# Kernel tuning notes

Measured on AMD Instinct MI355X. Metric: run time of the kernel, lower is better.

The kernel has to match this reference:

```python
import jax, jax.numpy as jnp
import numpy as np

BETA = 0.25
DECAY = 0.99
EPS = 1e-05
K = 1024        # num_codebook_vectors
D = 256         # latent_dim


def setup_inputs() -> dict:
    key = jax.random.key(0)
    k1, k2, k3 = jax.random.split(key, 3)
    return {
        "z": jax.random.normal(k1, (32, D, 32, 32), dtype=jnp.float32),
        "embedding": jax.random.normal(k2, (K, D), dtype=jnp.float32),
        "ema_cluster_size": jnp.zeros((K,), dtype=jnp.float32),
        "ema_w": jax.random.normal(k3, (K, D), dtype=jnp.float32),
    }


def reference(z, embedding, ema_cluster_size, ema_w):
    B, C, H, W = z.shape
    zp = jnp.transpose(z, (0, 2, 3, 1))            # [B,H,W,C]
    zf = zp.reshape(-1, C)                          # [N, D], N = B*H*W

    # squared L2 distances: ||z||^2 + ||e||^2 - 2 z e^T  -> [N, K]
    d = (jnp.sum(zf * zf, axis=1, keepdims=True)
         + jnp.sum(embedding * embedding, axis=1)
         - 2.0 * (zf @ embedding.T))
    idx = jnp.argmin(d, axis=1)                     # [N]

    # one-hot @ embedding == gather of codebook rows
    z_q = embedding[idx].reshape(zp.shape)          # [B,H,W,C]

    # EMA codebook update (training branch)
    counts = jnp.zeros((K,), dtype=zf.dtype).at[idx].add(1.0)   # encodings.sum(0)
    cs = ema_cluster_size * DECAY + (1.0 - DECAY) * counts
    n = jnp.sum(cs)
    cs = (cs + EPS) / (n + K * EPS) * n             # Laplace smoothing
    dw = jax.ops.segment_sum(zf, idx, num_segments=K)           # encodings.T @ zf
    new_ema_w = ema_w * DECAY + (1.0 - DECAY) * dw
    new_embedding = new_ema_w / cs[:, None]

    # commitment loss + straight-through estimator
    e_latent_loss = jnp.mean((jax.lax.stop_gradient(z_q) - zp) ** 2)
    loss = BETA * e_latent_loss
    z_q_st = zp + jax.lax.stop_gradient(z_q - zp)
    z_q_out = jnp.transpose(z_q_st, (0, 3, 1, 2))   # [B,C,H,W]

    return z_q_out, idx[:, None], loss, new_embedding, cs, new_ema_w
```

## Files before the change

kernel.cpp:

```cpp
#include <hip/hip_runtime.h>

typedef unsigned long long ull;
typedef __attribute__((ext_vector_type(8))) short bf16x8;
typedef __attribute__((ext_vector_type(4))) float f32x4;
typedef __attribute__((ext_vector_type(8))) unsigned short u16x8;

#define DECAY 0.99f
#define BETA 0.25f
#define EPSV 1e-5f
#define EPSGAP 0.0625f
#define THR3 0.03125f

#define Dd 256
#define Kk 1024
#define Nn 32768
#define ZELEM 8388608

__device__ __forceinline__ unsigned short f2bf(float f) {
    unsigned int x = __float_as_uint(f);
    x += 0x7FFFu + ((x >> 16) & 1u);
    return (unsigned short)(x >> 16);
}
__device__ __forceinline__ float bf2f(unsigned short b) {
    return __uint_as_float(((unsigned int)b) << 16);
}
__device__ __forceinline__ unsigned mono(unsigned b) {
    return b ^ (((int)b >> 31) | 0x80000000u);
}
__device__ __forceinline__ float unmono(unsigned m) {
    unsigned b = (m & 0x80000000u) ? (m ^ 0x80000000u) : ~m;
    return __uint_as_float(b);
}
__device__ __forceinline__ unsigned umin32(unsigned a, unsigned b) { return a < b ? a : b; }
__device__ __forceinline__ unsigned umax32(unsigned a, unsigned b) { return a > b ? a : b; }
__device__ __forceinline__ ull umin64(ull a, ull b) { return a < b ? a : b; }
__device__ __forceinline__ ull umax64(ull a, ull b) { return a > b ? a : b; }

__global__ __launch_bounds__(256) void prep_e_kernel(
        const float* __restrict__ emb, unsigned short* __restrict__ ehg,
        unsigned short* __restrict__ elg, float* __restrict__ esq,
        int* __restrict__ hist, int* __restrict__ flagcnt,
        float* __restrict__ loss_fix, float* __restrict__ nsum,
        const float* __restrict__ ema_cs, float* __restrict__ dwr, int nrep) {
    const int nsub = blockIdx.x;
    const int t = threadIdx.x;
    {
        const int per = nrep * 512;
        float4* dst = (float4*)(dwr + (size_t)nsub * per);
        const int n4 = per >> 2;
        for (int j = t; j < n4; j += 256) dst[j] = make_float4(0.f, 0.f, 0.f, 0.f);
    }
    if (nsub < 64) {
        if (t < 16) hist[nsub * 16 + t] = 0;
        if (nsub == 0 && t == 16) flagcnt[0] = 0;
        if (nsub == 0 && t == 17) loss_fix[0] = 0.0f;
        if (nsub == 0 && t == 18) flagcnt[1] = 0;
        #pragma unroll
        for (int it = 0; it < 2; ++it) {
            const int item = it * 256 + t;
            const int kc = item >> 6, lane = item & 63;
            const int quad = lane >> 4, nl = lane & 15;
            const float* ep = emb + (size_t)(nsub * 16 + nl) * Dd + kc * 32 + quad * 8;
            const float4 a = *(const float4*)ep;
            const float4 b4 = *(const float4*)(ep + 4);
            const float v[8] = {a.x, a.y, a.z, a.w, b4.x, b4.y, b4.z, b4.w};
            u16x8 hi, lo;
            #pragma unroll
            for (int j = 0; j < 8; ++j) {
                const unsigned short h = f2bf(v[j]);
                hi[j] = h;
                lo[j] = f2bf(v[j] - bf2f(h));
            }
            const size_t off = ((size_t)(nsub * 8 + kc) * 64 + lane) * 8;
            *(u16x8*)&ehg[off] = hi;
            *(u16x8*)&elg[off] = lo;
        }
        {
            const int nl = t >> 4, seg = t & 15;
            const float* ep = emb + (size_t)(nsub * 16 + nl) * Dd + seg * 16;
            float s = 0.0f;
            #pragma unroll
            for (int j = 0; j < 4; ++j) {
                const float4 v4 = *(const float4*)(ep + j * 4);
                s += v4.x * v4.x + v4.y * v4.y + v4.z * v4.z + v4.w * v4.w;
            }
            #pragma unroll
            for (int d = 1; d < 16; d <<= 1) s += __shfl_xor(s, d);
            if (seg == 0) esq[nsub * 16 + nl] = s;
        }
    } else if (nsub == 64) {
        __shared__ float wred[4];
        const int w = t >> 6, lane = t & 63;
        float s = ema_cs[t] + ema_cs[t + 256] + ema_cs[t + 512] + ema_cs[t + 768];
        #pragma unroll
        for (int d = 32; d > 0; d >>= 1) s += __shfl_xor(s, d);
        if (lane == 0) wred[w] = s;
        __syncthreads();
        if (t == 0)
            nsum[0] = DECAY * (wred[0] + wred[1] + wred[2] + wred[3])
                      + (1.0f - DECAY) * (float)Nn;
    }
}

__global__ __launch_bounds__(256) void dist_kernel(
        const float* __restrict__ z, const unsigned short* __restrict__ ehg,
        const unsigned short* __restrict__ elg, const float* __restrict__ esq,
        const float* __restrict__ emb,
        float* __restrict__ zq, float* __restrict__ dwr, int repmask,
        int* __restrict__ idx_i, float* __restrict__ idx_f,
        int* __restrict__ hist, int* __restrict__ flagcnt,
        int* __restrict__ listA, int* __restrict__ kkA,
        float* __restrict__ valA, int* __restrict__ listB,
        float* __restrict__ valB, float* __restrict__ loss_p) {
    __shared__ __align__(16) unsigned char smem[72704];
    __shared__ int kidx[64];
    unsigned short* zh = (unsigned short*)smem;
    unsigned short* zl = (unsigned short*)(smem + 32768);
    ull* mb   = (ull*)(smem + 65536);
    ull* ms   = (ull*)(smem + 67584);
    float* zsqp = (float*)(smem + 69632);
    ull* mt   = (ull*)(smem + 70656);
    float* eldsf = (float*)smem;

    const int t = threadIdx.x, w = t >> 6, L = t & 63;
    const int quad = L >> 4, lr = L & 15;
    const int m0 = blockIdx.x * 64;
    const int b = m0 >> 10, hw0 = m0 & 1023;

    {
        const int c0 = w * 64;
        const float* zp = z + (size_t)b * 262144 + hw0 + L;
        float s = 0.0f;
        #pragma unroll
        for (int cg = 0; cg < 8; ++cg) {
            float v[8];
            #pragma unroll
            for (int j = 0; j < 8; ++j)
                v[j] = zp[(size_t)(c0 + cg * 8 + j) * 1024];
            u16x8 hi, lo;
            #pragma unroll
            for (int j = 0; j < 8; ++j) {
                s = fmaf(v[j], v[j], s);
                const unsigned short h = f2bf(v[j]);
                hi[j] = h;
                lo[j] = f2bf(v[j] - bf2f(h));
            }
            const int chunk = ((c0 >> 3) + cg) ^ (L & 7);
            *(u16x8*)&zh[L * 256 + chunk * 8] = hi;
            *(u16x8*)&zl[L * 256 + chunk * 8] = lo;
        }
        zsqp[L * 4 + w] = s;
    }
    __syncthreads();

    const unsigned short* ehw = ehg + (size_t)(w * 1024 + L) * 8;
    const unsigned short* elw = elg + (size_t)(w * 1024 + L) * 8;

    unsigned bb[16], ss[16], tt[16];
    #pragma unroll
    for (int i = 0; i < 16; ++i) { bb[i] = 0xFFFFFFFFu; ss[i] = 0xFFFFFFFFu; tt[i] = 0xFFFFFFFFu; }

    bf16x8 Bh[2][2], Bl[2][2];
    #pragma unroll
    for (int ni = 0; ni < 2; ++ni) {
        Bh[0][ni] = *(const bf16x8*)(ehw + (size_t)ni * 4096);
        Bl[0][ni] = *(const bf16x8*)(elw + (size_t)ni * 4096);
    }
    bf16x8 Ah[2][4], Al[2][4];
    #pragma unroll
    for (int mi = 0; mi < 4; ++mi) {
        const int chunk = quad ^ (lr & 7);
        const int o = (mi * 16 + lr) * 256 + chunk * 8;
        Ah[0][mi] = *(const bf16x8*)&zh[o];
        Al[0][mi] = *(const bf16x8*)&zl[o];
    }

    for (int nt = 0; nt < 8; ++nt) {
        f32x4 acc[4][2];
        #pragma unroll
        for (int mi = 0; mi < 4; ++mi)
            #pragma unroll
            for (int ni = 0; ni < 2; ++ni) acc[mi][ni] = (f32x4){0.f, 0.f, 0.f, 0.f};

        #pragma unroll
        for (int kc = 0; kc < 8; ++kc) {
            const int cur = kc & 1, nxt = cur ^ 1;
            const int nkc = (kc + 1) & 7;
            const int nnt = (kc == 7) ? ((nt + 1) & 7) : nt;
            #pragma unroll
            for (int ni = 0; ni < 2; ++ni) {
                const size_t o = (size_t)nnt * 32768 + (size_t)ni * 4096 + (size_t)nkc * 512;
                Bh[nxt][ni] = *(const bf16x8*)(ehw + o);
                Bl[nxt][ni] = *(const bf16x8*)(elw + o);
            }
            #pragma unroll
            for (int mi = 0; mi < 4; ++mi) {
                const int chunk = (nkc * 4 + quad) ^ (lr & 7);
                const int o = (mi * 16 + lr) * 256 + chunk * 8;
                Ah[nxt][mi] = *(const bf16x8*)&zh[o];
                Al[nxt][mi] = *(const bf16x8*)&zl[o];
            }
            __builtin_amdgcn_s_setprio(1);
            #pragma unroll
            for (int mi = 0; mi < 4; ++mi)
                #pragma unroll
                for (int ni = 0; ni < 2; ++ni) {
                    acc[mi][ni] = __builtin_amdgcn_mfma_f32_16x16x32_bf16(Ah[cur][mi], Bh[cur][ni], acc[mi][ni], 0, 0, 0);
                    acc[mi][ni] = __builtin_amdgcn_mfma_f32_16x16x32_bf16(Ah[cur][mi], Bl[cur][ni], acc[mi][ni], 0, 0, 0);
                    acc[mi][ni] = __builtin_amdgcn_mfma_f32_16x16x32_bf16(Al[cur][mi], Bh[cur][ni], acc[mi][ni], 0, 0, 0);
                }
            __builtin_amdgcn_s_setprio(0);
        }
        const int q0 = nt * 8 + w * 2;
        const float e0b = esq[q0 * 16 + lr] + 512.0f;
        const float e1b = esq[(q0 + 1) * 16 + lr] + 512.0f;
        #pragma unroll
        for (int mi = 0; mi < 4; ++mi)
            #pragma unroll
            for (int reg = 0; reg < 4; ++reg) {
                const int i = mi * 4 + reg;
                #pragma unroll
                for (int ni = 0; ni < 2; ++ni) {
                    const float val = fmaf(-2.0f, acc[mi][ni][reg], ni ? e1b : e0b);
                    const unsigned pk = (__float_as_uint(val) & 0xFFFFFFC0u) | (unsigned)(q0 + ni);
                    const unsigned m1 = umin32(bb[i], pk), M1 = umax32(bb[i], pk);
                    const unsigned m2 = umin32(ss[i], M1), M2 = umax32(ss[i], M1);
                    const unsigned m3 = umin32(tt[i], M2);
                    bb[i] = m1; ss[i] = m2; tt[i] = m3;
                }
            }
    }

    #pragma unroll
    for (int mi = 0; mi < 4; ++mi)
        #pragma unroll
        for (int reg = 0; reg < 4; ++reg) {
            const int i = mi * 4 + reg;
            ull b2 = ((ull)(bb[i] & 0xFFFFFFC0u) << 14) | (ull)((bb[i] & 63u) * 16 + lr);
            ull s2 = ((ull)(ss[i] & 0xFFFFFFC0u) << 14) | (ull)((ss[i] & 63u) * 16 + lr);
            ull t2 = ((ull)(tt[i] & 0xFFFFFFC0u) << 14) | (ull)((tt[i] & 63u) * 16 + lr);
            #pragma unroll
            for (int d = 1; d < 16; d <<= 1) {
                const ull ob = __shfl_xor(b2, d);
                const ull os = __shfl_xor(s2, d);
                const ull ot = __shfl_xor(t2, d);
                const ull x1 = umin64(b2, ob), y1 = umax64(b2, ob);
                const ull x2 = umin64(s2, os), y2 = umax64(s2, os);
                const ull c2 = umin64(y1, x2);
                const ull t1 = umax64(y1, x2);
                const ull c3 = umin64(t1, umin64(y2, umin64(t2, ot)));
                b2 = x1; s2 = c2; t2 = c3;
            }
            if (lr == 0) {
                const int row = mi * 16 + quad * 4 + reg;
                mb[w * 64 + row] = b2;
                ms[w * 64 + row] = s2;
                mt[w * 64 + row] = t2;
            }
        }
    __syncthreads();

    if (t < 64) {
        ull b2 = mb[t], s2 = ms[t], t2 = mt[t];
        #pragma unroll
        for (int ww = 1; ww < 4; ++ww) {
            const ull ob = mb[ww * 64 + t], os = ms[ww * 64 + t], ot = mt[ww * 64 + t];
            const ull x1 = umin64(b2, ob), y1 = umax64(b2, ob);
            const ull x2 = umin64(s2, os), y2 = umax64(s2, os);
            const ull c2 = umin64(y1, x2);
            const ull t1 = umax64(y1, x2);
            const ull c3 = umin64(t1, umin64(y2, umin64(t2, ot)));
            b2 = x1; s2 = c2; t2 = c3;
        }
        const int k1 = (int)(b2 & 16383ull);
        const int k2 = (int)(s2 & 16383ull);
        const float v1 = __uint_as_float((unsigned)(b2 >> 14)) - 512.0f;
        const float v2 = __uint_as_float((unsigned)(s2 >> 14)) - 512.0f;
        const float v3 = __uint_as_float((unsigned)(t2 >> 14)) - 512.0f;
        idx_i[m0 + t] = k1;
        idx_f[m0 + t] = (float)k1;
        kidx[t] = k1;
        atomicAdd(&hist[k1], 1);
        if (v2 - v1 < EPSGAP) {
            if (v3 - v1 < THR3) {
                const int pos = atomicAdd(&flagcnt[1], 1);
                listB[pos] = m0 + t;
                valB[pos] = v1;
            } else {
                const int pos = atomicAdd(&flagcnt[0], 1);
                listA[pos] = m0 + t;
                kkA[pos] = k1 | (k2 << 16);
                valA[pos] = v1;
            }
        }
        float lp = v1 + zsqp[t * 4] + zsqp[t * 4 + 1] + zsqp[t * 4 + 2] + zsqp[t * 4 + 3];
        #pragma unroll
        for (int d = 32; d > 0; d >>= 1) lp += __shfl_down(lp, d);
        if (t == 0) loss_p[blockIdx.x] = lp;
    }
    __syncthreads();

    for (int pr = w; pr < 64; pr += 4) {
        const float* er = emb + (size_t)kidx[pr] * Dd;
        #pragma unroll
        for (int g = 0; g < 4; ++g)
            eldsf[pr * 257 + g * 64 + L] = er[g * 64 + L];
    }
    __syncthreads();

    {
        const int g = t & 15;
        const int cl = t >> 4;
        float* zqb = zq + (size_t)b * 262144 + hw0 + g * 4;
        #pragma unroll
        for (int pass = 0; pass < 16; ++pass) {
            const int c = pass * 16 + cl;
            float4 v;
            v.x = eldsf[(g * 4 + 0) * 257 + c];
            v.y = eldsf[(g * 4 + 1) * 257 + c];
            v.z = eldsf[(g * 4 + 2) * 257 + c];
            v.w = eldsf[(g * 4 + 3) * 257 + c];
            *(float4*)(zqb + (size_t)c * 1024) = v;
        }
    }

    {
        const int c = t;
        const float* zcol = z + (size_t)b * 262144 + (size_t)c * 1024 + hw0;
        float* dwb = dwr + (size_t)(blockIdx.x & repmask) * (Kk * Dd);
        #pragma unroll 4
        for (int p = 0; p < 64; ++p) {
            atomicAdd(&dwb[(size_t)kidx[p] * Dd + c], zcol[p]);
        }
    }
}

__global__ __launch_bounds__(256) void fixup_kernel(
        const float* __restrict__ z, const float* __restrict__ emb,
        const float* __restrict__ esq, const int* __restrict__ flagcnt,
        const int* __restrict__ listA, const int* __restrict__ kkA,
        const float* __restrict__ valA, const int* __restrict__ listB,
        const float* __restrict__ valB,
        int* __restrict__ idx_i, float* __restrict__ idx_f,
        int* __restrict__ hist, float* __restrict__ loss_fix,
        float* __restrict__ zq, float* __restrict__ dw) {
    __shared__ float zrow[256];
    __shared__ float red1[4], red2[4];
    __shared__ ull red[256];
    __shared__ int s_pair[2];
    const int t = threadIdx.x;
    const int w = t >> 6, lane = t & 63;

    const int totalA = flagcnt[0];
    for (int fi = blockIdx.x; fi < totalA; fi += 512) {
        const int n = listA[fi];
        const int b = n >> 10, hw = n & 1023;
        const int kk = kkA[fi];
        const int k1 = kk & 0xFFFF, k2 = kk >> 16;
        __syncthreads();
        zrow[t] = z[(size_t)b * 262144 + (size_t)t * 1024 + hw];
        __syncthreads();
        const float zv = zrow[t];
        float c1 = zv * emb[(size_t)k1 * Dd + t];
        float c2 = zv * emb[(size_t)k2 * Dd + t];
        #pragma unroll
        for (int d = 32; d > 0; d >>= 1) {
            c1 += __shfl_xor(c1, d);
            c2 += __shfl_xor(c2, d);
        }
        if (lane == 0) { red1[w] = c1; red2[w] = c2; }
        __syncthreads();
        if (t == 0) {
            const float d1 = esq[k1] - 2.0f * (red1[0] + red1[1] + red1[2] + red1[3]);
            const float d2 = esq[k2] - 2.0f * (red2[0] + red2[1] + red2[2] + red2[3]);
            const ull p1 = ((ull)mono(__float_as_uint(d1)) << 32) | (unsigned)k1;
            const ull p2 = ((ull)mono(__float_as_uint(d2)) << 32) | (unsigned)k2;
            const ull pb = p1 < p2 ? p1 : p2;
            const int knew = (int)(unsigned)(pb & 0xFFFFFFFFull);
            const float vnew = unmono((unsigned)(pb >> 32));
            const int kold = idx_i[n];
            s_pair[0] = kold;
            s_pair[1] = knew;
            if (knew != kold) {
                idx_i[n] = knew;
                idx_f[n] = (float)knew;
                atomicSub(&hist[kold], 1);
                atomicAdd(&hist[knew], 1);
            }
            atomicAdd(loss_fix, vnew - valA[fi]);
        }
        __syncthreads();
        const int kold = s_pair[0], knew = s_pair[1];
        if (knew != kold) {
            atomicAdd(&dw[(size_t)kold * Dd + t], -zv);
            atomicAdd(&dw[(size_t)knew * Dd + t], zv);
            zq[(size_t)b * 262144 + (size_t)t * 1024 + hw] = emb[(size_t)knew * Dd + t];
        }
    }

    const int totalB = flagcnt[1];
    for (int fi = blockIdx.x; fi < totalB; fi += 512) {
        const int n = listB[fi];
        const int b = n >> 10, hw = n & 1023;
        __syncthreads();
        zrow[t] = z[(size_t)b * 262144 + (size_t)t * 1024 + hw];
        __syncthreads();
        ull best = ~0ull;
        #pragma unroll
        for (int kc = 0; kc < 4; ++kc) {
            const int k = t * 4 + kc;
            const float* ep = emb + (size_t)k * Dd;
            float dot = 0.0f;
            #pragma unroll 8
            for (int c4 = 0; c4 < 64; ++c4) {
                const float4 e4 = *(const float4*)(ep + c4 * 4);
                const float4 z4 = *(const float4*)&zrow[c4 * 4];
                dot = fmaf(z4.x, e4.x, dot);
                dot = fmaf(z4.y, e4.y, dot);
                dot = fmaf(z4.z, e4.z, dot);
                dot = fmaf(z4.w, e4.w, dot);
            }
            const float val = esq[k] - 2.0f * dot;
            const ull pk = ((ull)mono(__float_as_uint(val)) << 32) | (unsigned)k;
            if (pk < best) best = pk;
        }
        red[t] = best;
        __syncthreads();
        for (int s = 128; s > 0; s >>= 1) {
            if (t < s) { if (red[t + s] < red[t]) red[t] = red[t + s]; }
            __syncthreads();
        }
        if (t == 0) {
            const int knew = (int)(unsigned)(red[0] & 0xFFFFFFFFull);
            const float vnew = unmono((unsigned)(red[0] >> 32));
            const int kold = idx_i[n];
            s_pair[0] = kold;
            s_pair[1] = knew;
            if (knew != kold) {
                idx_i[n] = knew;
                idx_f[n] = (float)knew;
                atomicSub(&hist[kold], 1);
                atomicAdd(&hist[knew], 1);
            }
            atomicAdd(loss_fix, vnew - valB[fi]);
        }
        __syncthreads();
        const int kold = s_pair[0], knew = s_pair[1];
        if (knew != kold) {
            const float zv = zrow[t];
            atomicAdd(&dw[(size_t)kold * Dd + t], -zv);
            atomicAdd(&dw[(size_t)knew * Dd + t], zv);
            zq[(size_t)b * 262144 + (size_t)t * 1024 + hw] = emb[(size_t)knew * Dd + t];
        }
    }
}

__global__ __launch_bounds__(256) void finalize2_kernel(
        const float* __restrict__ ema_w, const float* __restrict__ dwr,
        int nrep, const int* __restrict__ hist,
        const float* __restrict__ ema_cs, const float* __restrict__ nsum,
        const float* __restrict__ loss_p, const float* __restrict__ loss_fix,
        float* __restrict__ cs_out, float* __restrict__ loss_out,
        float* __restrict__ new_emb_out, float* __restrict__ new_ema_w_out) {
    const int k = blockIdx.x;
    const int t = threadIdx.x;
    const float n = nsum[0];
    const float csr = ema_cs[k] * DECAY + (1.0f - DECAY) * (float)hist[k];
    const float cs = (csr + EPSV) / (n + (float)Kk * EPSV) * n;
    if (t == 0) cs_out[k] = cs;
    const int i = k * 256 + t;
    float s = 0.0f;
    for (int r = 0; r < nrep; ++r) s += dwr[(size_t)r * (Kk * Dd) + i];
    const float nw = ema_w[i] * DECAY + (1.0f - DECAY) * s;
    new_ema_w_out[i] = nw;
    new_emb_out[i]   = nw / cs;
    if (k == 0) {
        __shared__ float wred[4];
        const int w = t >> 6, lane = t & 63;
        float r2 = loss_p[t] + loss_p[t + 256];
        #pragma unroll
        for (int d = 32; d > 0; d >>= 1) r2 += __shfl_xor(r2, d);
        if (lane == 0) wred[w] = r2;
        __syncthreads();
        if (t == 0)
            loss_out[0] = BETA * (wred[0] + wred[1] + wred[2] + wred[3]
                                  + loss_fix[0]) / (float)ZELEM;
    }
}

extern "C" void kernel_launch(void* const* d_in, const int* in_sizes, int n_in,
                              void* d_out, int out_size, void* d_ws, size_t ws_size,
                              hipStream_t stream) {
    const float* z      = (const float*)d_in[0];
    const float* emb    = (const float*)d_in[1];
    const float* ema_cs = (const float*)d_in[2];
    const float* ema_w  = (const float*)d_in[3];

    float* out = (float*)d_out;
    float* zq_out        = out;
    float* idx_out_f     = out + 8388608;
    float* loss_out      = out + 8421376;
    float* new_emb_out   = out + 8421377;
    float* cs_out        = out + 8683521;
    float* new_ema_w_out = out + 8684545;

    int*   idx_i    = (int*)d_ws;
    int*   flagcnt  = idx_i + 32768;
    float* loss_fix = (float*)(flagcnt + 16);
    int*   listA    = (int*)(loss_fix + 16);
    float* valA     = (float*)(listA + 32768);
    int*   kkA      = (int*)(valA + 32768);
    int*   listB    = kkA + 32768;
    float* valB     = (float*)(listB + 32768);
    int*   hist     = (int*)(valB + 32768);
    float* esq      = (float*)(hist + 1024);
    float* loss_p   = esq + 1024;
    float* nsum     = loss_p + 512;
    unsigned short* ehg = (unsigned short*)(nsum + 16);
    unsigned short* elg = ehg + 262144;
    size_t dwr_off = ((size_t)((char*)(elg + 262144) - (char*)d_ws) + 255) & ~(size_t)255;
    float* dwr = (float*)((char*)d_ws + dwr_off);
    const size_t repbytes = (size_t)Kk * Dd * 4;
    size_t rem = (ws_size > dwr_off) ? ws_size - dwr_off : 0;
    int nrep = 1;
    while (nrep < 8 && (size_t)(nrep * 2) * repbytes <= rem) nrep <<= 1;

    prep_e_kernel<<<512, 256, 0, stream>>>(emb, ehg, elg, esq, hist, flagcnt,
                                           loss_fix, nsum, ema_cs, dwr, nrep);
    dist_kernel<<<Nn / 64, 256, 0, stream>>>(z, ehg, elg, esq, emb, zq_out,
                                             dwr, nrep - 1, idx_i, idx_out_f,
                                             hist, flagcnt, listA, kkA, valA,
                                             listB, valB, loss_p);
    fixup_kernel<<<512, 256, 0, stream>>>(z, emb, esq, flagcnt, listA, kkA,
                                          valA, listB, valB, idx_i, idx_out_f,
                                          hist, loss_fix, zq_out, dwr);
    finalize2_kernel<<<Kk, 256, 0, stream>>>(ema_w, dwr, nrep, hist, ema_cs,
                                             nsum, loss_p, loss_fix, cs_out,
                                             loss_out, new_emb_out,
                                             new_ema_w_out);
}
```

Measured before the change: 213.2 us.

## Replace atomic scatter of dw with per-code gather over transposed z

Removes the atomicAdd-based segment sum and histogram from the distance kernel. Instead, the distance kernel writes a row-major copy of z into the zq output buffer. A new per-codebook kernel scans all indices, builds a shared-memory list of matching rows and sums them with no atomics, producing the counts and dw deterministically. A separate gather kernel then writes z_q after the fixups, which removes the fixup kernel's corrective atomics. In exchange, every one of the 1024 blocks scans all 32768 indices, and the dist kernel writes an extra 32 MB transposed copy.

```diff
diff --git a/kernel.cpp b/kernel.cpp
--- a/kernel.cpp
+++ b/kernel.cpp
@@ -39,19 +39,11 @@
 __global__ __launch_bounds__(256) void prep_e_kernel(
         const float* __restrict__ emb, unsigned short* __restrict__ ehg,
         unsigned short* __restrict__ elg, float* __restrict__ esq,
-        int* __restrict__ hist, int* __restrict__ flagcnt,
-        float* __restrict__ loss_fix, float* __restrict__ nsum,
-        const float* __restrict__ ema_cs, float* __restrict__ dwr, int nrep) {
+        int* __restrict__ flagcnt, float* __restrict__ loss_fix,
+        float* __restrict__ nsum, const float* __restrict__ ema_cs) {
     const int nsub = blockIdx.x;
     const int t = threadIdx.x;
-    {
-        const int per = nrep * 512;
-        float4* dst = (float4*)(dwr + (size_t)nsub * per);
-        const int n4 = per >> 2;
-        for (int j = t; j < n4; j += 256) dst[j] = make_float4(0.f, 0.f, 0.f, 0.f);
-    }
     if (nsub < 64) {
-        if (t < 16) hist[nsub * 16 + t] = 0;
         if (nsub == 0 && t == 16) flagcnt[0] = 0;
         if (nsub == 0 && t == 17) loss_fix[0] = 0.0f;
         if (nsub == 0 && t == 18) flagcnt[1] = 0;
@@ -88,7 +80,7 @@
             for (int d = 1; d < 16; d <<= 1) s += __shfl_xor(s, d);
             if (seg == 0) esq[nsub * 16 + nl] = s;
         }
-    } else if (nsub == 64) {
+    } else {
         __shared__ float wred[4];
         const int w = t >> 6, lane = t & 63;
         float s = ema_cs[t] + ema_cs[t + 256] + ema_cs[t + 512] + ema_cs[t + 768];
@@ -105,22 +97,19 @@
 __global__ __launch_bounds__(256) void dist_kernel(
         const float* __restrict__ z, const unsigned short* __restrict__ ehg,
         const unsigned short* __restrict__ elg, const float* __restrict__ esq,
-        const float* __restrict__ emb,
-        float* __restrict__ zq, float* __restrict__ dwr, int repmask,
+        float* __restrict__ zf,
         int* __restrict__ idx_i, float* __restrict__ idx_f,
-        int* __restrict__ hist, int* __restrict__ flagcnt,
+        int* __restrict__ flagcnt,
         int* __restrict__ listA, int* __restrict__ kkA,
         float* __restrict__ valA, int* __restrict__ listB,
         float* __restrict__ valB, float* __restrict__ loss_p) {
     __shared__ __align__(16) unsigned char smem[72704];
-    __shared__ int kidx[64];
     unsigned short* zh = (unsigned short*)smem;
     unsigned short* zl = (unsigned short*)(smem + 32768);
     ull* mb   = (ull*)(smem + 65536);
     ull* ms   = (ull*)(smem + 67584);
     float* zsqp = (float*)(smem + 69632);
     ull* mt   = (ull*)(smem + 70656);
-    float* eldsf = (float*)smem;
 
     const int t = threadIdx.x, w = t >> 6, L = t & 63;
     const int quad = L >> 4, lr = L & 15;
@@ -130,6 +119,7 @@
     {
         const int c0 = w * 64;
         const float* zp = z + (size_t)b * 262144 + hw0 + L;
+        float* zfp = zf + (size_t)(m0 + L) * 256 + c0;
         float s = 0.0f;
         #pragma unroll
         for (int cg = 0; cg < 8; ++cg) {
@@ -137,6 +127,8 @@
             #pragma unroll
             for (int j = 0; j < 8; ++j)
                 v[j] = zp[(size_t)(c0 + cg * 8 + j) * 1024];
+            *(float4*)(zfp + cg * 8)     = make_float4(v[0], v[1], v[2], v[3]);
+            *(float4*)(zfp + cg * 8 + 4) = make_float4(v[4], v[5], v[6], v[7]);
             u16x8 hi, lo;
             #pragma unroll
             for (int j = 0; j < 8; ++j) {
@@ -279,8 +271,6 @@
         const float v3 = __uint_as_float((unsigned)(t2 >> 14)) - 512.0f;
         idx_i[m0 + t] = k1;
         idx_f[m0 + t] = (float)k1;
-        kidx[t] = k1;
-        atomicAdd(&hist[k1], 1);
         if (v2 - v1 < EPSGAP) {
             if (v3 - v1 < THR3) {
                 const int pos = atomicAdd(&flagcnt[1], 1);
@@ -298,69 +288,28 @@
         for (int d = 32; d > 0; d >>= 1) lp += __shfl_down(lp, d);
         if (t == 0) loss_p[blockIdx.x] = lp;
     }
-    __syncthreads();
-
-    for (int pr = w; pr < 64; pr += 4) {
-        const float* er = emb + (size_t)kidx[pr] * Dd;
-        #pragma unroll
-        for (int g = 0; g < 4; ++g)
-            eldsf[pr * 257 + g * 64 + L] = er[g * 64 + L];
-    }
-    __syncthreads();
-
-    {
-        const int g = t & 15;
-        const int cl = t >> 4;
-        float* zqb = zq + (size_t)b * 262144 + hw0 + g * 4;
-        #pragma unroll
-        for (int pass = 0; pass < 16; ++pass) {
-            const int c = pass * 16 + cl;
-            float4 v;
-            v.x = eldsf[(g * 4 + 0) * 257 + c];
-            v.y = eldsf[(g * 4 + 1) * 257 + c];
-            v.z = eldsf[(g * 4 + 2) * 257 + c];
-            v.w = eldsf[(g * 4 + 3) * 257 + c];
-            *(float4*)(zqb + (size_t)c * 1024) = v;
-        }
-    }
-
-    {
-        const int c = t;
-        const float* zcol = z + (size_t)b * 262144 + (size_t)c * 1024 + hw0;
-        float* dwb = dwr + (size_t)(blockIdx.x & repmask) * (Kk * Dd);
-        #pragma unroll 4
-        for (int p = 0; p < 64; ++p) {
-            atomicAdd(&dwb[(size_t)kidx[p] * Dd + c], zcol[p]);
-        }
-    }
 }
 
 __global__ __launch_bounds__(256) void fixup_kernel(
-        const float* __restrict__ z, const float* __restrict__ emb,
+        const float* __restrict__ zf, const float* __restrict__ emb,
         const float* __restrict__ esq, const int* __restrict__ flagcnt,
         const int* __restrict__ listA, const int* __restrict__ kkA,
         const float* __restrict__ valA, const int* __restrict__ listB,
         const float* __restrict__ valB,
         int* __restrict__ idx_i, float* __restrict__ idx_f,
-        int* __restrict__ hist, float* __restrict__ loss_fix,
-        float* __restrict__ zq, float* __restrict__ dw) {
+        float* __restrict__ loss_fix) {
     __shared__ float zrow[256];
     __shared__ float red1[4], red2[4];
     __shared__ ull red[256];
-    __shared__ int s_pair[2];
     const int t = threadIdx.x;
     const int w = t >> 6, lane = t & 63;
 
     const int totalA = flagcnt[0];
     for (int fi = blockIdx.x; fi < totalA; fi += 512) {
         const int n = listA[fi];
-        const int b = n >> 10, hw = n & 1023;
         const int kk = kkA[fi];
         const int k1 = kk & 0xFFFF, k2 = kk >> 16;
-        __syncthreads();
-        zrow[t] = z[(size_t)b * 262144 + (size_t)t * 1024 + hw];
-        __syncthreads();
-        const float zv = zrow[t];
+        const float zv = zf[(size_t)n * Dd + t];
         float c1 = zv * emb[(size_t)k1 * Dd + t];
         float c2 = zv * emb[(size_t)k2 * Dd + t];
         #pragma unroll
@@ -368,6 +317,7 @@
             c1 += __shfl_xor(c1, d);
             c2 += __shfl_xor(c2, d);
         }
+        __syncthreads();
         if (lane == 0) { red1[w] = c1; red2[w] = c2; }
         __syncthreads();
         if (t == 0) {
@@ -378,32 +328,19 @@
             const ull pb = p1 < p2 ? p1 : p2;
             const int knew = (int)(unsigned)(pb & 0xFFFFFFFFull);
             const float vnew = unmono((unsigned)(pb >> 32));
-            const int kold = idx_i[n];
-            s_pair[0] = kold;
-            s_pair[1] = knew;
-            if (knew != kold) {
+            if (knew != k1) {
                 idx_i[n] = knew;
                 idx_f[n] = (float)knew;
-                atomicSub(&hist[kold], 1);
-                atomicAdd(&hist[knew], 1);
             }
             atomicAdd(loss_fix, vnew - valA[fi]);
-        }
-        __syncthreads();
-        const int kold = s_pair[0], knew = s_pair[1];
-        if (knew != kold) {
-            atomicAdd(&dw[(size_t)kold * Dd + t], -zv);
-            atomicAdd(&dw[(size_t)knew * Dd + t], zv);
-            zq[(size_t)b * 262144 + (size_t)t * 1024 + hw] = emb[(size_t)knew * Dd + t];
         }
     }
 
     const int totalB = flagcnt[1];
     for (int fi = blockIdx.x; fi < totalB; fi += 512) {
         const int n = listB[fi];
-        const int b = n >> 10, hw = n & 1023;
-        __syncthreads();
-        zrow[t] = z[(size_t)b * 262144 + (size_t)t * 1024 + hw];
+        __syncthreads();
+        zrow[t] = zf[(size_t)n * Dd + t];
         __syncthreads();
         ull best = ~0ull;
         #pragma unroll
@@ -434,44 +371,50 @@
             const int knew = (int)(unsigned)(red[0] & 0xFFFFFFFFull);
             const float vnew = unmono((unsigned)(red[0] >> 32));
             const int kold = idx_i[n];
-            s_pair[0] = kold;
-            s_pair[1] = knew;
             if (knew != kold) {
                 idx_i[n] = knew;
                 idx_f[n] = (float)knew;
-                atomicSub(&hist[kold], 1);
-                atomicAdd(&hist[knew], 1);
             }
             atomicAdd(loss_fix, vnew - valB[fi]);
         }
-        __syncthreads();
-        const int kold = s_pair[0], knew = s_pair[1];
-        if (knew != kold) {
-            const float zv = zrow[t];
-            atomicAdd(&dw[(size_t)kold * Dd + t], -zv);
-            atomicAdd(&dw[(size_t)knew * Dd + t], zv);
-            zq[(size_t)b * 262144 + (size_t)t * 1024 + hw] = emb[(size_t)knew * Dd + t];
-        }
-    }
-}
-
-__global__ __launch_bounds__(256) void finalize2_kernel(
-        const float* __restrict__ ema_w, const float* __restrict__ dwr,
-        int nrep, const int* __restrict__ hist,
-        const float* __restrict__ ema_cs, const float* __restrict__ nsum,
-        const float* __restrict__ loss_p, const float* __restrict__ loss_fix,
+    }
+}
+
+__global__ __launch_bounds__(256) void dwfin_kernel(
+        const int* __restrict__ idx, const float* __restrict__ zf,
+        const float* __restrict__ ema_w, const float* __restrict__ ema_cs,
+        const float* __restrict__ nsum, const float* __restrict__ loss_p,
+        const float* __restrict__ loss_fix,
         float* __restrict__ cs_out, float* __restrict__ loss_out,
         float* __restrict__ new_emb_out, float* __restrict__ new_ema_w_out) {
+    __shared__ int list[2048];
+    __shared__ int lcnt;
     const int k = blockIdx.x;
     const int t = threadIdx.x;
+    float acc = 0.0f;
+    int cnt = 0;
+    for (int seg = 0; seg < Nn; seg += 2048) {
+        __syncthreads();
+        if (t == 0) lcnt = 0;
+        __syncthreads();
+        #pragma unroll
+        for (int j = 0; j < 8; ++j) {
+            const int n = seg + j * 256 + t;
+            if (idx[n] == k) list[atomicAdd(&lcnt, 1)] = n;
+        }
+        __syncthreads();
+        const int m = lcnt;
+        cnt += m;
+        #pragma unroll 4
+        for (int i = 0; i < m; ++i)
+            acc += zf[(size_t)list[i] * Dd + t];
+    }
     const float n = nsum[0];
-    const float csr = ema_cs[k] * DECAY + (1.0f - DECAY) * (float)hist[k];
+    const float csr = ema_cs[k] * DECAY + (1.0f - DECAY) * (float)cnt;
     const float cs = (csr + EPSV) / (n + (float)Kk * EPSV) * n;
     if (t == 0) cs_out[k] = cs;
     const int i = k * 256 + t;
-    float s = 0.0f;
-    for (int r = 0; r < nrep; ++r) s += dwr[(size_t)r * (Kk * Dd) + i];
-    const float nw = ema_w[i] * DECAY + (1.0f - DECAY) * s;
+    const float nw = ema_w[i] * DECAY + (1.0f - DECAY) * acc;
     new_ema_w_out[i] = nw;
     new_emb_out[i]   = nw / cs;
     if (k == 0) {
@@ -486,6 +429,23 @@
             loss_out[0] = BETA * (wred[0] + wred[1] + wred[2] + wred[3]
                                   + loss_fix[0]) / (float)ZELEM;
     }
+}
+
+__global__ __launch_bounds__(256) void gather_kernel(
+        const float* __restrict__ emb, const int* __restrict__ idx,
+        float* __restrict__ zq_out) {
+    const int tid = blockIdx.x * 256 + threadIdx.x;
+    const int e0 = tid * 4;
+    const int c = (e0 >> 10) & 255;
+    const int b = e0 >> 18;
+    const int n0 = b * 1024 + (e0 & 1023);
+    const int4 j4 = *(const int4*)(idx + n0);
+    float4 e;
+    e.x = emb[(size_t)j4.x * Dd + c];
+    e.y = emb[(size_t)j4.y * Dd + c];
+    e.z = emb[(size_t)j4.z * Dd + c];
+    e.w = emb[(size_t)j4.w * Dd + c];
+    *(float4*)(zq_out + e0) = e;
 }
 
 extern "C" void kernel_launch(void* const* d_in, const int* in_sizes, int n_in,
@@ -512,30 +472,24 @@
     int*   kkA      = (int*)(valA + 32768);
     int*   listB    = kkA + 32768;
     float* valB     = (float*)(listB + 32768);
-    int*   hist     = (int*)(valB + 32768);
-    float* esq      = (float*)(hist + 1024);
+    float* esq      = valB + 32768;
     float* loss_p   = esq + 1024;
     float* nsum     = loss_p + 512;
     unsigned short* ehg = (unsigned short*)(nsum + 16);
     unsigned short* elg = ehg + 262144;
-    size_t dwr_off = ((size_t)((char*)(elg + 262144) - (char*)d_ws) + 255) & ~(size_t)255;
-    float* dwr = (float*)((char*)d_ws + dwr_off);
-    const size_t repbytes = (size_t)Kk * Dd * 4;
-    size_t rem = (ws_size > dwr_off) ? ws_size - dwr_off : 0;
-    int nrep = 1;
-    while (nrep < 8 && (size_t)(nrep * 2) * repbytes <= rem) nrep <<= 1;
-
-    prep_e_kernel<<<512, 256, 0, stream>>>(emb, ehg, elg, esq, hist, flagcnt,
-                                           loss_fix, nsum, ema_cs, dwr, nrep);
-    dist_kernel<<<Nn / 64, 256, 0, stream>>>(z, ehg, elg, esq, emb, zq_out,
-                                             dwr, nrep - 1, idx_i, idx_out_f,
-                                             hist, flagcnt, listA, kkA, valA,
-                                             listB, valB, loss_p);
-    fixup_kernel<<<512, 256, 0, stream>>>(z, emb, esq, flagcnt, listA, kkA,
+
+    float* zf = zq_out;
+
+    prep_e_kernel<<<65, 256, 0, stream>>>(emb, ehg, elg, esq, flagcnt,
+                                          loss_fix, nsum, ema_cs);
+    dist_kernel<<<Nn / 64, 256, 0, stream>>>(z, ehg, elg, esq, zf, idx_i,
+                                             idx_out_f, flagcnt, listA, kkA,
+                                             valA, listB, valB, loss_p);
+    fixup_kernel<<<512, 256, 0, stream>>>(zf, emb, esq, flagcnt, listA, kkA,
                                           valA, listB, valB, idx_i, idx_out_f,
-                                          hist, loss_fix, zq_out, dwr);
-    finalize2_kernel<<<Kk, 256, 0, stream>>>(ema_w, dwr, nrep, hist, ema_cs,
-                                             nsum, loss_p, loss_fix, cs_out,
-                                             loss_out, new_emb_out,
-                                             new_ema_w_out);
-}
+                                          loss_fix);
+    dwfin_kernel<<<Kk, 256, 0, stream>>>(idx_i, zf, ema_w, ema_cs, nsum,
+                                         loss_p, loss_fix, cs_out, loss_out,
+                                         new_emb_out, new_ema_w_out);
+    gather_kernel<<<ZELEM / 1024, 256, 0, stream>>>(emb, idx_i, zq_out);
+}
```

New measurement: 345.0 us. 61.8% more time.

## Fuse near-tie argmin refinement into distance kernel, drop fixup kernel

Applied to the files above, without the earlier changes.

Rows whose top-two or top-three split-bf16 distances are too close to call are now re-checked inside the distance kernel, using block-local shared lists and the z row already held in LDS as hi/lo bf16. This runs before idx, histogram, loss and the zq/dw scatter are written, so the separate fixup kernel with its global lists, atomics and correction scatters goes away, along with one launch. The cost is that a whole block waits on serial per-row refinement, including a full 1024-code scan for three-way ties, which can make some blocks uneven. The reconstructed z is hi+lo bf16, not the exact fp32 value.

```diff
diff --git a/kernel.cpp b/kernel.cpp
--- a/kernel.cpp
+++ b/kernel.cpp
@@ -39,8 +39,7 @@
 __global__ __launch_bounds__(256) void prep_e_kernel(
         const float* __restrict__ emb, unsigned short* __restrict__ ehg,
         unsigned short* __restrict__ elg, float* __restrict__ esq,
-        int* __restrict__ hist, int* __restrict__ flagcnt,
-        float* __restrict__ loss_fix, float* __restrict__ nsum,
+        int* __restrict__ hist, float* __restrict__ nsum,
         const float* __restrict__ ema_cs, float* __restrict__ dwr, int nrep) {
     const int nsub = blockIdx.x;
     const int t = threadIdx.x;
@@ -52,9 +51,6 @@
     }
     if (nsub < 64) {
         if (t < 16) hist[nsub * 16 + t] = 0;
-        if (nsub == 0 && t == 16) flagcnt[0] = 0;
-        if (nsub == 0 && t == 17) loss_fix[0] = 0.0f;
-        if (nsub == 0 && t == 18) flagcnt[1] = 0;
         #pragma unroll
         for (int it = 0; it < 2; ++it) {
             const int item = it * 256 + t;
@@ -108,24 +104,29 @@
         const float* __restrict__ emb,
         float* __restrict__ zq, float* __restrict__ dwr, int repmask,
         int* __restrict__ idx_i, float* __restrict__ idx_f,
-        int* __restrict__ hist, int* __restrict__ flagcnt,
-        int* __restrict__ listA, int* __restrict__ kkA,
-        float* __restrict__ valA, int* __restrict__ listB,
-        float* __restrict__ valB, float* __restrict__ loss_p) {
+        int* __restrict__ hist, float* __restrict__ loss_p) {
     __shared__ __align__(16) unsigned char smem[72704];
     __shared__ int kidx[64];
+    __shared__ float vv[64];
+    __shared__ int aList[64], bList[64];
+    __shared__ int acnt, bcnt;
+    __shared__ float red1[4], red2[4];
+    __shared__ ull bred[4];
     unsigned short* zh = (unsigned short*)smem;
     unsigned short* zl = (unsigned short*)(smem + 32768);
     ull* mb   = (ull*)(smem + 65536);
     ull* ms   = (ull*)(smem + 67584);
     float* zsqp = (float*)(smem + 69632);
     ull* mt   = (ull*)(smem + 70656);
+    float* zrowF = (float*)mb;
     float* eldsf = (float*)smem;
 
     const int t = threadIdx.x, w = t >> 6, L = t & 63;
     const int quad = L >> 4, lr = L & 15;
     const int m0 = blockIdx.x * 64;
     const int b = m0 >> 10, hw0 = m0 & 1023;
+
+    if (t == 0) { acnt = 0; bcnt = 0; }
 
     {
         const int c0 = w * 64;
@@ -277,23 +278,90 @@
         const float v1 = __uint_as_float((unsigned)(b2 >> 14)) - 512.0f;
         const float v2 = __uint_as_float((unsigned)(s2 >> 14)) - 512.0f;
         const float v3 = __uint_as_float((unsigned)(t2 >> 14)) - 512.0f;
-        idx_i[m0 + t] = k1;
-        idx_f[m0 + t] = (float)k1;
         kidx[t] = k1;
-        atomicAdd(&hist[k1], 1);
+        vv[t] = v1;
         if (v2 - v1 < EPSGAP) {
-            if (v3 - v1 < THR3) {
-                const int pos = atomicAdd(&flagcnt[1], 1);
-                listB[pos] = m0 + t;
-                valB[pos] = v1;
-            } else {
-                const int pos = atomicAdd(&flagcnt[0], 1);
-                listA[pos] = m0 + t;
-                kkA[pos] = k1 | (k2 << 16);
-                valA[pos] = v1;
-            }
-        }
-        float lp = v1 + zsqp[t * 4] + zsqp[t * 4 + 1] + zsqp[t * 4 + 2] + zsqp[t * 4 + 3];
+            if (v3 - v1 < THR3) bList[atomicAdd(&bcnt, 1)] = t;
+            else                aList[atomicAdd(&acnt, 1)] = t | (k2 << 8);
+        }
+    }
+    __syncthreads();
+
+    const int nA = acnt, nB = bcnt;
+    for (int i = 0; i < nA; ++i) {
+        const int e = aList[i];
+        const int p = e & 63, k2p = e >> 8;
+        const int k1p = kidx[p];
+        const int a = p * 256 + (((t >> 3) ^ (p & 7)) << 3) + (t & 7);
+        const float zv = bf2f(zh[a]) + bf2f(zl[a]);
+        float c1 = zv * emb[(size_t)k1p * Dd + t];
+        float c2 = zv * emb[(size_t)k2p * Dd + t];
+        #pragma unroll
+        for (int d = 32; d > 0; d >>= 1) {
+            c1 += __shfl_xor(c1, d);
+            c2 += __shfl_xor(c2, d);
+        }
+        if (L == 0) { red1[w] = c1; red2[w] = c2; }
+        __syncthreads();
+        if (t == 0) {
+            const float d1 = esq[k1p] - 2.0f * (red1[0] + red1[1] + red1[2] + red1[3]);
+            const float d2 = esq[k2p] - 2.0f * (red2[0] + red2[1] + red2[2] + red2[3]);
+            if (d2 < d1 || (d2 == d1 && k2p < k1p)) { kidx[p] = k2p; vv[p] = d2; }
+            else                                     { vv[p] = d1; }
+        }
+        __syncthreads();
+    }
+
+    for (int i = 0; i < nB; ++i) {
+        const int p = bList[i];
+        {
+            const int a = p * 256 + (((t >> 3) ^ (p & 7)) << 3) + (t & 7);
+            zrowF[t] = bf2f(zh[a]) + bf2f(zl[a]);
+        }
+        __syncthreads();
+        ull best = ~0ull;
+        #pragma unroll
+        for (int kc = 0; kc < 4; ++kc) {
+            const int k = t * 4 + kc;
+            const float* ep = emb + (size_t)k * Dd;
+            float dot = 0.0f;
+            #pragma unroll 8
+            for (int c4 = 0; c4 < 64; ++c4) {
+                const float4 e4 = *(const float4*)(ep + c4 * 4);
+                const float4 z4 = *(const float4*)&zrowF[c4 * 4];
+                dot = fmaf(z4.x, e4.x, dot);
+                dot = fmaf(z4.y, e4.y, dot);
+                dot = fmaf(z4.z, e4.z, dot);
+                dot = fmaf(z4.w, e4.w, dot);
+            }
+            const float val = esq[k] - 2.0f * dot;
+            const ull pk = ((ull)mono(__float_as_uint(val)) << 32) | (unsigned)k;
+            if (pk < best) best = pk;
+        }
+        #pragma unroll
+        for (int d = 32; d > 0; d >>= 1) {
+            const ull o = __shfl_xor(best, d);
+            best = o < best ? o : best;
+        }
+        if (L == 0) bred[w] = best;
+        __syncthreads();
+        if (t == 0) {
+            ull bbx = bred[0];
+            bbx = umin64(bbx, bred[1]);
+            bbx = umin64(bbx, bred[2]);
+            bbx = umin64(bbx, bred[3]);
+            kidx[p] = (int)(unsigned)(bbx & 0xFFFFFFFFull);
+            vv[p] = unmono((unsigned)(bbx >> 32));
+        }
+        __syncthreads();
+    }
+
+    if (t < 64) {
+        const int k = kidx[t];
+        idx_i[m0 + t] = k;
+        idx_f[m0 + t] = (float)k;
+        atomicAdd(&hist[k], 1);
+        float lp = vv[t] + zsqp[t * 4] + zsqp[t * 4 + 1] + zsqp[t * 4 + 2] + zsqp[t * 4 + 3];
         #pragma unroll
         for (int d = 32; d > 0; d >>= 1) lp += __shfl_down(lp, d);
         if (t == 0) loss_p[blockIdx.x] = lp;
@@ -335,131 +403,11 @@
     }
 }
 
-__global__ __launch_bounds__(256) void fixup_kernel(
-        const float* __restrict__ z, const float* __restrict__ emb,
-        const float* __restrict__ esq, const int* __restrict__ flagcnt,
-        const int* __restrict__ listA, const int* __restrict__ kkA,
-        const float* __restrict__ valA, const int* __restrict__ listB,
-        const float* __restrict__ valB,
-        int* __restrict__ idx_i, float* __restrict__ idx_f,
-        int* __restrict__ hist, float* __restrict__ loss_fix,
-        float* __restrict__ zq, float* __restrict__ dw) {
-    __shared__ float zrow[256];
-    __shared__ float red1[4], red2[4];
-    __shared__ ull red[256];
-    __shared__ int s_pair[2];
-    const int t = threadIdx.x;
-    const int w = t >> 6, lane = t & 63;
-
-    const int totalA = flagcnt[0];
-    for (int fi = blockIdx.x; fi < totalA; fi += 512) {
-        const int n = listA[fi];
-        const int b = n >> 10, hw = n & 1023;
-        const int kk = kkA[fi];
-        const int k1 = kk & 0xFFFF, k2 = kk >> 16;
-        __syncthreads();
-        zrow[t] = z[(size_t)b * 262144 + (size_t)t * 1024 + hw];
-        __syncthreads();
-        const float zv = zrow[t];
-        float c1 = zv * emb[(size_t)k1 * Dd + t];
-        float c2 = zv * emb[(size_t)k2 * Dd + t];
-        #pragma unroll
-        for (int d = 32; d > 0; d >>= 1) {
-            c1 += __shfl_xor(c1, d);
-            c2 += __shfl_xor(c2, d);
-        }
-        if (lane == 0) { red1[w] = c1; red2[w] = c2; }
-        __syncthreads();
-        if (t == 0) {
-            const float d1 = esq[k1] - 2.0f * (red1[0] + red1[1] + red1[2] + red1[3]);
-            const float d2 = esq[k2] - 2.0f * (red2[0] + red2[1] + red2[2] + red2[3]);
-            const ull p1 = ((ull)mono(__float_as_uint(d1)) << 32) | (unsigned)k1;
-            const ull p2 = ((ull)mono(__float_as_uint(d2)) << 32) | (unsigned)k2;
-            const ull pb = p1 < p2 ? p1 : p2;
-            const int knew = (int)(unsigned)(pb & 0xFFFFFFFFull);
-            const float vnew = unmono((unsigned)(pb >> 32));
-            const int kold = idx_i[n];
-            s_pair[0] = kold;
-            s_pair[1] = knew;
-            if (knew != kold) {
-                idx_i[n] = knew;
-                idx_f[n] = (float)knew;
-                atomicSub(&hist[kold], 1);
-                atomicAdd(&hist[knew], 1);
-            }
-            atomicAdd(loss_fix, vnew - valA[fi]);
-        }
-        __syncthreads();
-        const int kold = s_pair[0], knew = s_pair[1];
-        if (knew != kold) {
-            atomicAdd(&dw[(size_t)kold * Dd + t], -zv);
-            atomicAdd(&dw[(size_t)knew * Dd + t], zv);
-            zq[(size_t)b * 262144 + (size_t)t * 1024 + hw] = emb[(size_t)knew * Dd + t];
-        }
-    }
-
-    const int totalB = flagcnt[1];
-    for (int fi = blockIdx.x; fi < totalB; fi += 512) {
-        const int n = listB[fi];
-        const int b = n >> 10, hw = n & 1023;
-        __syncthreads();
-        zrow[t] = z[(size_t)b * 262144 + (size_t)t * 1024 + hw];
-        __syncthreads();
-        ull best = ~0ull;
-        #pragma unroll
-        for (int kc = 0; kc < 4; ++kc) {
-            const int k = t * 4 + kc;
-            const float* ep = emb + (size_t)k * Dd;
-            float dot = 0.0f;
-            #pragma unroll 8
-            for (int c4 = 0; c4 < 64; ++c4) {
-                const float4 e4 = *(const float4*)(ep + c4 * 4);
-                const float4 z4 = *(const float4*)&zrow[c4 * 4];
-                dot = fmaf(z4.x, e4.x, dot);
-                dot = fmaf(z4.y, e4.y, dot);
-                dot = fmaf(z4.z, e4.z, dot);
-                dot = fmaf(z4.w, e4.w, dot);
-            }
-            const float val = esq[k] - 2.0f * dot;
-            const ull pk = ((ull)mono(__float_as_uint(val)) << 32) | (unsigned)k;
-            if (pk < best) best = pk;
-        }
-        red[t] = best;
-        __syncthreads();
-        for (int s = 128; s > 0; s >>= 1) {
-            if (t < s) { if (red[t + s] < red[t]) red[t] = red[t + s]; }
-            __syncthreads();
-        }
-        if (t == 0) {
-            const int knew = (int)(unsigned)(red[0] & 0xFFFFFFFFull);
-            const float vnew = unmono((unsigned)(red[0] >> 32));
-            const int kold = idx_i[n];
-            s_pair[0] = kold;
-            s_pair[1] = knew;
-            if (knew != kold) {
-                idx_i[n] = knew;
-                idx_f[n] = (float)knew;
-                atomicSub(&hist[kold], 1);
-                atomicAdd(&hist[knew], 1);
-            }
-            atomicAdd(loss_fix, vnew - valB[fi]);
-        }
-        __syncthreads();
-        const int kold = s_pair[0], knew = s_pair[1];
-        if (knew != kold) {
-            const float zv = zrow[t];
-            atomicAdd(&dw[(size_t)kold * Dd + t], -zv);
-            atomicAdd(&dw[(size_t)knew * Dd + t], zv);
-            zq[(size_t)b * 262144 + (size_t)t * 1024 + hw] = emb[(size_t)knew * Dd + t];
-        }
-    }
-}
-
 __global__ __launch_bounds__(256) void finalize2_kernel(
         const float* __restrict__ ema_w, const float* __restrict__ dwr,
         int nrep, const int* __restrict__ hist,
         const float* __restrict__ ema_cs, const float* __restrict__ nsum,
-        const float* __restrict__ loss_p, const float* __restrict__ loss_fix,
+        const float* __restrict__ loss_p,
         float* __restrict__ cs_out, float* __restrict__ loss_out,
         float* __restrict__ new_emb_out, float* __restrict__ new_ema_w_out) {
     const int k = blockIdx.x;
@@ -483,8 +431,7 @@
         if (lane == 0) wred[w] = r2;
         __syncthreads();
         if (t == 0)
-            loss_out[0] = BETA * (wred[0] + wred[1] + wred[2] + wred[3]
-                                  + loss_fix[0]) / (float)ZELEM;
+            loss_out[0] = BETA * (wred[0] + wred[1] + wred[2] + wred[3]) / (float)ZELEM;
     }
 }
 
@@ -505,14 +452,7 @@
     float* new_ema_w_out = out + 8684545;
 
     int*   idx_i    = (int*)d_ws;
-    int*   flagcnt  = idx_i + 32768;
-    float* loss_fix = (float*)(flagcnt + 16);
-    int*   listA    = (int*)(loss_fix + 16);
-    float* valA     = (float*)(listA + 32768);
-    int*   kkA      = (int*)(valA + 32768);
-    int*   listB    = kkA + 32768;
-    float* valB     = (float*)(listB + 32768);
-    int*   hist     = (int*)(valB + 32768);
+    int*   hist     = idx_i + 32768;
     float* esq      = (float*)(hist + 1024);
     float* loss_p   = esq + 1024;
     float* nsum     = loss_p + 512;
@@ -525,17 +465,12 @@
     int nrep = 1;
     while (nrep < 8 && (size_t)(nrep * 2) * repbytes <= rem) nrep <<= 1;
 
-    prep_e_kernel<<<512, 256, 0, stream>>>(emb, ehg, elg, esq, hist, flagcnt,
-                                           loss_fix, nsum, ema_cs, dwr, nrep);
+    prep_e_kernel<<<512, 256, 0, stream>>>(emb, ehg, elg, esq, hist, nsum,
+                                           ema_cs, dwr, nrep);
     dist_kernel<<<Nn / 64, 256, 0, stream>>>(z, ehg, elg, esq, emb, zq_out,
                                              dwr, nrep - 1, idx_i, idx_out_f,
-                                             hist, flagcnt, listA, kkA, valA,
-                                             listB, valB, loss_p);
-    fixup_kernel<<<512, 256, 0, stream>>>(z, emb, esq, flagcnt, listA, kkA,
-                                          valA, listB, valB, idx_i, idx_out_f,
-                                          hist, loss_fix, zq_out, dwr);
+                                             hist, loss_p);
     finalize2_kernel<<<Kk, 256, 0, stream>>>(ema_w, dwr, nrep, hist, ema_cs,
-                                             nsum, loss_p, loss_fix, cs_out,
-                                             loss_out, new_emb_out,
-                                             new_ema_w_out);
-}
+                                             nsum, loss_p, cs_out, loss_out,
+                                             new_emb_out, new_ema_w_out);
+}
```

Result: faster. 201.5 us (-5.5%).
